# Optimization experiments

Measured on AMD Instinct MI355X. Metric: run time of the kernel, lower is better.

The kernel has to match this reference:

```python
import jax, jax.numpy as jnp
import numpy as np
from jax import lax

DN = ('NCHW', 'OIHW', 'NCHW')

def conv2d(x, w, b):
    y = lax.conv_general_dilated(x, w, (1, 1), 'SAME', dimension_numbers=DN)
    return y + b[None, :, None, None]


def setup_inputs() -> dict:
    key = jax.random.key(0)
    ks = jax.random.split(key, 12)
    B, H, W = 16, 256, 256
    def wt(k, shape):
        return jax.random.normal(k, shape, jnp.float32) * 0.05
    return {
        'x': jax.random.normal(ks[0], (B, 1, H, W), jnp.float32),
        'g': jax.random.normal(ks[1], (B, 1, H, W), jnp.float32),
        # conv1 branch (x): 1->64 relu 64->1
        'w1a': wt(ks[2], (64, 1, 3, 3)), 'b1a': jnp.zeros((64,), jnp.float32),
        'w1b': wt(ks[3], (1, 64, 3, 3)), 'b1b': jnp.zeros((1,), jnp.float32),
        # conv2 branch (g): 1->64 relu 64->1
        'w2a': wt(ks[4], (64, 1, 3, 3)), 'b2a': jnp.zeros((64,), jnp.float32),
        'w2b': wt(ks[5], (1, 64, 3, 3)), 'b2b': jnp.zeros((1,), jnp.float32),
        # dynamic filter head: 2->64 relu 64->64 relu 64->81, softmax over taps
        'wfa': wt(ks[6], (64, 2, 3, 3)), 'bfa': jnp.zeros((64,), jnp.float32),
        'wfb': wt(ks[7], (64, 64, 3, 3)), 'bfb': jnp.zeros((64,), jnp.float32),
        'wfc': wt(ks[8], (81, 64, 3, 3)), 'bfc': jnp.zeros((81,), jnp.float32),
    }


def reference(x, g, w1a, b1a, w1b, b1b, w2a, b2a, w2b, b2b,
              wfa, bfa, wfb, bfb, wfc, bfc):
    # feature branches -> 1 channel each
    x_ = conv2d(jax.nn.relu(conv2d(x, w1a, b1a)), w1b, b1b)   # [B,1,H,W]
    g_ = conv2d(jax.nn.relu(conv2d(g, w2a, b2a)), w2b, b2b)   # [B,1,H,W]
    feat = jnp.concatenate([x_, g_], axis=1)                   # [B,2,H,W]
    # per-pixel 9x9 dynamic filter (81 taps), softmax-normalized
    h = jax.nn.relu(conv2d(feat, wfa, bfa))
    h = jax.nn.relu(conv2d(h, wfb, bfb))
    filt = jax.nn.softmax(conv2d(h, wfc, bfc), axis=1)         # [B,81,H,W]
    # unfold: 9x9 neighborhoods with zero pad 4, row-major tap order
    # matches torch unfold(2,9,1).unfold(3,9,1).permute(0,1,4,5,2,3)
    patches = lax.conv_general_dilated_patches(
        x, (9, 9), (1, 1), padding=((4, 4), (4, 4)),
        dimension_numbers=DN)                                  # [B,81,H,W]
    out = jnp.sum(patches * filt, axis=1, keepdims=True)       # [B,1,H,W]
    return out
```

## Files before the change

kernel.cpp:

```cpp
#include <hip/hip_runtime.h>

#define NB 16
#define HH 256
#define WW 256
#define NPIX (HH*WW)
#define LOG2E 1.44269504088896f

typedef _Float16 f16;
typedef _Float16 f16x8 __attribute__((ext_vector_type(8)));
typedef float f32x4 __attribute__((ext_vector_type(4)));

__device__ __forceinline__ int swzoff(int p, int c) {
    return p * 64 + ((((c >> 3) ^ (p & 7)) << 3) | (c & 7));
}

__global__ __launch_bounds__(256) void prepack_kernel(
    const float* __restrict__ w1a, const float* __restrict__ w2a,
    const float* __restrict__ w1b, const float* __restrict__ w2b,
    const float* __restrict__ wfa, const float* __restrict__ wfb,
    const float* __restrict__ wfc,
    f16* __restrict__ pA1, f16* __restrict__ pA2, f16* __restrict__ pWa,
    f16* __restrict__ pBs1, f16* __restrict__ pBs2,
    f16* __restrict__ pWbF, f16* __restrict__ pWcF)
{
    int i = blockIdx.x * 256 + threadIdx.x;
    if (i < 2048) {
        int c = i >> 5, k = i & 31;
        pA1[i] = (f16)(k < 9 ? w1a[c * 9 + k] : 0.f);
        pA2[i] = (f16)(k < 9 ? w2a[c * 9 + k] : 0.f);
        pWa[i] = (f16)(k < 18 ? wfa[c * 18 + k] : 0.f);
    }
    if (i < 1024) {
        int r = i >> 6, cin = i & 63;
        pBs1[i] = (f16)(r < 9 ? w1b[cin * 9 + r] : 0.f);
        pBs2[i] = (f16)(r < 9 ? w2b[cin * 9 + r] : 0.f);
    }
    if (i < 36864) {
        int kk = i / 2048, r = i & 2047;
        int mt = r >> 9, e = r & 511;
        int l = e >> 3, j = e & 7;
        int cout = mt * 16 + (l & 15);
        int k = kk * 32 + ((l >> 4) << 3) + j;
        int tap = k >> 6, cin = k & 63;
        pWbF[i] = (f16)wfb[(cout * 64 + cin) * 9 + tap];
    }
    if (i < 55296) {
        int kk = i / 3072, r = i % 3072;
        int mt = r >> 9, e = r & 511;
        int l = e >> 3, j = e & 7;
        int cout = mt * 16 + (l & 15);
        int k = kk * 32 + ((l >> 4) << 3) + j;
        int tap = k >> 6, cin = k & 63;
        pWcF[i] = (f16)(cout < 81 ? wfc[(cout * 64 + cin) * 9 + tap] * LOG2E : 0.f);
    }
}

__global__ __launch_bounds__(256, 3) void k1_branch(
    const float* __restrict__ x, const float* __restrict__ g,
    const float* __restrict__ b1a, const float* __restrict__ b2a,
    const float* __restrict__ b1b, const float* __restrict__ b2b,
    const f16* __restrict__ pA1, const f16* __restrict__ pA2,
    const f16* __restrict__ pBs1, const f16* __restrict__ pBs2,
    float* __restrict__ feat)
{
    __shared__ f16 xt[400];
    __shared__ f16 hid[20736];
    __shared__ f16 part[9 * 328];
    __shared__ float bA[64];

    const int tid = threadIdx.x;
    const int wid = tid >> 6, lane = tid & 63;
    const int gq = lane >> 4, cl = lane & 15;
    const int x0 = blockIdx.x * 16, y0 = blockIdx.y * 16;
    const int b = blockIdx.z >> 1, br = blockIdx.z & 1;

    const float* in = (br ? g : x) + (size_t)b * NPIX;
    const f16* pA = br ? pA2 : pA1;
    const f16* pBs = br ? pBs2 : pBs1;
    const float bscal = (br ? b2b : b1b)[0];

    for (int t = tid; t < 400; t += 256) {
        int r = t / 20, c = t % 20;
        int gy = y0 - 2 + r, gx = x0 - 2 + c;
        xt[t] = (f16)(((unsigned)gy < (unsigned)HH && (unsigned)gx < (unsigned)WW)
                          ? in[gy * WW + gx] : 0.f);
    }
    if (tid < 64) bA[tid] = (br ? b2a : b1a)[tid];

    int koff[8];
    #pragma unroll
    for (int j = 0; j < 8; j++) {
        int k = gq * 8 + j;
        int kc = k < 9 ? k : 0;
        koff[j] = (kc / 3) * 20 + (kc % 3);
    }

    f16x8 afA[4];
    #pragma unroll
    for (int mt = 0; mt < 4; mt++)
        afA[mt] = *(const f16x8*)&pA[(mt * 16 + cl) * 32 + gq * 8];
    f16x8 afS0 = *(const f16x8*)&pBs[cl * 64 + gq * 8];
    f16x8 afS1 = *(const f16x8*)&pBs[cl * 64 + 32 + gq * 8];
    __syncthreads();

    #pragma unroll
    for (int it = 0; it < 6; it++) {
        int nt = wid + it * 4;
        if (nt < 21) {
            int p = nt * 16 + cl;
            int pc = p > 323 ? 323 : p;
            int py = pc / 18, px = pc - 18 * py;
            int base = py * 20 + px;
            f16x8 bf;
            #pragma unroll
            for (int j = 0; j < 8; j++) bf[j] = xt[base + koff[j]];
            int gy = y0 - 1 + py, gx = x0 - 1 + px;
            bool ok = (p < 324) &&
                      ((unsigned)gy < (unsigned)HH && (unsigned)gx < (unsigned)WW);
            #pragma unroll
            for (int mt = 0; mt < 4; mt++) {
                f32x4 z = {0.f, 0.f, 0.f, 0.f};
                f32x4 acc = __builtin_amdgcn_mfma_f32_16x16x32_f16(afA[mt], bf, z, 0, 0, 0);
                if (p < 324) {
                    int c0 = mt * 16 + gq * 4;
                    union { f16 h[4]; uint2 u2; } pk;
                    #pragma unroll
                    for (int r = 0; r < 4; r++)
                        pk.h[r] = (f16)(ok ? fmaxf(acc[r] + bA[c0 + r], 0.f) : 0.f);
                    *(uint2*)&hid[swzoff(p, c0)] = pk.u2;
                }
            }
        }
    }
    __syncthreads();

    #pragma unroll
    for (int it = 0; it < 6; it++) {
        int nt = wid + it * 4;
        if (nt < 21) {
            int p = nt * 16 + cl;
            int pc = p > 323 ? 323 : p;
            f16x8 bf0 = *(const f16x8*)&hid[swzoff(pc, gq * 8)];
            f16x8 bf1 = *(const f16x8*)&hid[swzoff(pc, 32 + gq * 8)];
            f32x4 z = {0.f, 0.f, 0.f, 0.f};
            f32x4 d = __builtin_amdgcn_mfma_f32_16x16x32_f16(afS0, bf0, z, 0, 0, 0);
            d = __builtin_amdgcn_mfma_f32_16x16x32_f16(afS1, bf1, d, 0, 0, 0);
            #pragma unroll
            for (int r = 0; r < 4; r++) {
                int tap = gq * 4 + r;
                if (tap < 9 && p < 324)
                    part[tap * 328 + p] = (f16)d[r];
            }
        }
    }
    __syncthreads();

    {
        int ty = tid >> 4, tx = tid & 15;
        float s = bscal;
        #pragma unroll
        for (int u = 0; u < 3; u++)
            #pragma unroll
            for (int v = 0; v < 3; v++)
                s += (float)part[(u * 3 + v) * 328 + (ty + u) * 18 + tx + v];
        feat[((size_t)(b * 2 + br)) * NPIX + (y0 + ty) * WW + x0 + tx] = s;
    }
}

__global__ __launch_bounds__(256, 3) void k2_wfab(
    const float* __restrict__ feat, const f16* __restrict__ pWa,
    const f16* __restrict__ pWbF, const float* __restrict__ bfa,
    const float* __restrict__ bfb, f16* __restrict__ h2g, int b0)
{
    __shared__ f16 ftt[800];
    __shared__ f16 hid[20736];
    __shared__ float bA[64];
    __shared__ float bB[64];

    const int tid = threadIdx.x;
    const int wid = tid >> 6, lane = tid & 63;
    const int gq = lane >> 4, cl = lane & 15;
    const int x0 = blockIdx.x * 16, y0 = blockIdx.y * 16;
    const int ci = blockIdx.z, b = b0 + ci;

    for (int t = tid; t < 800; t += 256) {
        int cin = t / 400, p = t - 400 * cin;
        int r = p / 20, c = p - 20 * r;
        int gy = y0 - 2 + r, gx = x0 - 2 + c;
        ftt[t] = (f16)(((unsigned)gy < (unsigned)HH && (unsigned)gx < (unsigned)WW)
                           ? feat[((size_t)(b * 2 + cin)) * NPIX + gy * WW + gx] : 0.f);
    }
    if (tid < 64) { bA[tid] = bfa[tid]; bB[tid] = bfb[tid]; }

    int koff[8];
    #pragma unroll
    for (int j = 0; j < 8; j++) {
        int k = gq * 8 + j;
        int kc = k < 18 ? k : 0;
        int cin = kc >= 9 ? 1 : 0;
        int tap = kc - 9 * cin;
        koff[j] = cin * 400 + (tap / 3) * 20 + (tap % 3);
    }

    f16x8 afW[4];
    #pragma unroll
    for (int mt = 0; mt < 4; mt++)
        afW[mt] = *(const f16x8*)&pWa[(mt * 16 + cl) * 32 + gq * 8];
    __syncthreads();

    #pragma unroll
    for (int it = 0; it < 6; it++) {
        int nt = wid + it * 4;
        if (nt < 21) {
            int p = nt * 16 + cl;
            int pc = p > 323 ? 323 : p;
            int py = pc / 18, px = pc - 18 * py;
            int base = py * 20 + px;
            f16x8 bf;
            #pragma unroll
            for (int j = 0; j < 8; j++) bf[j] = ftt[base + koff[j]];
            int gy = y0 - 1 + py, gx = x0 - 1 + px;
            bool ok = (p < 324) &&
                      ((unsigned)gy < (unsigned)HH && (unsigned)gx < (unsigned)WW);
            #pragma unroll
            for (int mt = 0; mt < 4; mt++) {
                f32x4 z = {0.f, 0.f, 0.f, 0.f};
                f32x4 acc = __builtin_amdgcn_mfma_f32_16x16x32_f16(afW[mt], bf, z, 0, 0, 0);
                if (p < 324) {
                    int c0 = mt * 16 + gq * 4;
                    union { f16 h[4]; uint2 u2; } pk;
                    #pragma unroll
                    for (int r = 0; r < 4; r++)
                        pk.h[r] = (f16)(ok ? fmaxf(acc[r] + bA[c0 + r], 0.f) : 0.f);
                    *(uint2*)&hid[swzoff(p, c0)] = pk.u2;
                }
            }
        }
    }
    __syncthreads();

    f32x4 acc[4][4];
    #pragma unroll
    for (int i = 0; i < 4; i++)
        #pragma unroll
        for (int mt = 0; mt < 4; mt++) acc[i][mt] = (f32x4){0.f, 0.f, 0.f, 0.f};

    int pre_i[4];
    #pragma unroll
    for (int i = 0; i < 4; i++) pre_i[i] = (wid * 4 + i) * 18 + cl;
    const int A0 = gq * 8;
    const int A1 = 32 + gq * 8;

    const f16* wfp = pWbF + (size_t)lane * 8;
    f16x8 afA[4], afB[4];
    #pragma unroll
    for (int mt = 0; mt < 4; mt++)
        afA[mt] = *(const f16x8*)&wfp[mt * 512];

    #pragma unroll 1
    for (int kt = 0; kt < 9; kt++) {
        int u = kt / 3, duv = u * 18 + (kt - 3 * u);
        #pragma unroll
        for (int mt = 0; mt < 4; mt++)
            afB[mt] = *(const f16x8*)&wfp[((2 * kt + 1) * 4 + mt) * 512];
        #pragma unroll
        for (int i = 0; i < 4; i++) {
            int p = pre_i[i] + duv;
            f16x8 bf = *(const f16x8*)&hid[(p << 6) + (A0 ^ ((p & 7) << 3))];
            __builtin_amdgcn_s_setprio(1);
            #pragma unroll
            for (int mt = 0; mt < 4; mt++)
                acc[i][mt] = __builtin_amdgcn_mfma_f32_16x16x32_f16(afA[mt], bf, acc[i][mt], 0, 0, 0);
            __builtin_amdgcn_s_setprio(0);
        }
        if (kt < 8) {
            #pragma unroll
            for (int mt = 0; mt < 4; mt++)
                afA[mt] = *(const f16x8*)&wfp[((2 * kt + 2) * 4 + mt) * 512];
        }
        #pragma unroll
        for (int i = 0; i < 4; i++) {
            int p = pre_i[i] + duv;
            f16x8 bf = *(const f16x8*)&hid[(p << 6) + (A1 ^ ((p & 7) << 3))];
            __builtin_amdgcn_s_setprio(1);
            #pragma unroll
            for (int mt = 0; mt < 4; mt++)
                acc[i][mt] = __builtin_amdgcn_mfma_f32_16x16x32_f16(afB[mt], bf, acc[i][mt], 0, 0, 0);
            __builtin_amdgcn_s_setprio(0);
        }
    }
    #pragma unroll
    for (int i = 0; i < 4; i++) {
        int nt = wid * 4 + i;
        size_t pb = ((size_t)ci * NPIX + (size_t)((y0 + nt) * WW + x0 + cl)) * 64;
        #pragma unroll
        for (int mt = 0; mt < 4; mt++) {
            int c0 = mt * 16 + gq * 4;
            union { f16 h[4]; uint2 u2; } pk;
            #pragma unroll
            for (int r = 0; r < 4; r++)
                pk.h[r] = (f16)fmaxf(acc[i][mt][r] + bB[c0 + r], 0.f);
            *(uint2*)&h2g[pb + c0] = pk.u2;
        }
    }
}

__global__ __launch_bounds__(256, 3) void k3_wfc_apply(
    const f16* __restrict__ h2g, const f16* __restrict__ pWcF,
    const float* __restrict__ bfc, const float* __restrict__ x,
    float* __restrict__ out, int b0)
{
    __shared__ f16 h2t[20736];
    __shared__ float xt24[576];
    __shared__ float bC[96];

    const int tid = threadIdx.x;
    const int wid = tid >> 6, lane = tid & 63;
    const int gq = lane >> 4, cl = lane & 15;
    const int x0 = blockIdx.x * 16, y0 = blockIdx.y * 16;
    const int ci = blockIdx.z, b = b0 + ci;

    for (int t = tid; t < 2592; t += 256) {
        int p = t >> 3, grp = t & 7;
        int py = p / 18, px = p - 18 * py;
        int gy = y0 - 1 + py, gx = x0 - 1 + px;
        f16x8 v = {};
        if ((unsigned)gy < (unsigned)HH && (unsigned)gx < (unsigned)WW)
            v = *(const f16x8*)&h2g[((size_t)ci * NPIX + (size_t)(gy * WW + gx)) * 64 + grp * 8];
        *(f16x8*)&h2t[swzoff(p, grp * 8)] = v;
    }
    const float* xb = x + (size_t)b * NPIX;
    for (int t = tid; t < 576; t += 256) {
        int r = t / 24, c = t - 24 * r;
        int gy = y0 - 4 + r, gx = x0 - 4 + c;
        xt24[t] = ((unsigned)gy < (unsigned)HH && (unsigned)gx < (unsigned)WW)
                      ? xb[gy * WW + gx] : 0.f;
    }
    if (tid < 96) bC[tid] = tid < 81 ? bfc[tid] * LOG2E : -1e30f;
    __syncthreads();

    f32x4 acc[4][6];
    #pragma unroll
    for (int i = 0; i < 4; i++)
        #pragma unroll
        for (int mt = 0; mt < 6; mt++) acc[i][mt] = (f32x4){0.f, 0.f, 0.f, 0.f};

    int pre_i[4];
    #pragma unroll
    for (int i = 0; i < 4; i++) pre_i[i] = (wid * 4 + i) * 18 + cl;
    const int A0 = gq * 8;
    const int A1 = 32 + gq * 8;

    const f16* wfp = pWcF + (size_t)lane * 8;
    f16x8 afA[6], afB[6];
    #pragma unroll
    for (int mt = 0; mt < 6; mt++)
        afA[mt] = *(const f16x8*)&wfp[mt * 512];

    #pragma unroll 1
    for (int kt = 0; kt < 9; kt++) {
        int u = kt / 3, duv = u * 18 + (kt - 3 * u);
        #pragma unroll
        for (int mt = 0; mt < 6; mt++)
            afB[mt] = *(const f16x8*)&wfp[((2 * kt + 1) * 6 + mt) * 512];
        #pragma unroll
        for (int i = 0; i < 4; i++) {
            int p = pre_i[i] + duv;
            f16x8 bf = *(const f16x8*)&h2t[(p << 6) + (A0 ^ ((p & 7) << 3))];
            __builtin_amdgcn_s_setprio(1);
            #pragma unroll
            for (int mt = 0; mt < 6; mt++)
                acc[i][mt] = __builtin_amdgcn_mfma_f32_16x16x32_f16(afA[mt], bf, acc[i][mt], 0, 0, 0);
            __builtin_amdgcn_s_setprio(0);
        }
        if (kt < 8) {
            #pragma unroll
            for (int mt = 0; mt < 6; mt++)
                afA[mt] = *(const f16x8*)&wfp[((2 * kt + 2) * 6 + mt) * 512];
        }
        #pragma unroll
        for (int i = 0; i < 4; i++) {
            int p = pre_i[i] + duv;
            f16x8 bf = *(const f16x8*)&h2t[(p << 6) + (A1 ^ ((p & 7) << 3))];
            __builtin_amdgcn_s_setprio(1);
            #pragma unroll
            for (int mt = 0; mt < 6; mt++)
                acc[i][mt] = __builtin_amdgcn_mfma_f32_16x16x32_f16(afB[mt], bf, acc[i][mt], 0, 0, 0);
            __builtin_amdgcn_s_setprio(0);
        }
    }

    int xoff[6][4];
    #pragma unroll
    for (int mt = 0; mt < 6; mt++)
        #pragma unroll
        for (int r = 0; r < 4; r++) {
            int c = mt * 16 + gq * 4 + r;
            xoff[mt][r] = (c / 9) * 24 + (c % 9);
        }

    #pragma unroll
    for (int i = 0; i < 4; i++) {
        int nt = wid * 4 + i;
        int xbase = nt * 24 + cl;
        float val[6][4];
        float m = -1e30f;
        #pragma unroll
        for (int mt = 0; mt < 6; mt++)
            #pragma unroll
            for (int r = 0; r < 4; r++) {
                int c = mt * 16 + gq * 4 + r;
                float vv = acc[i][mt][r] + bC[c];
                val[mt][r] = vv;
                m = fmaxf(m, vv);
            }
        m = fmaxf(m, __shfl_xor(m, 16));
        m = fmaxf(m, __shfl_xor(m, 32));
        float s = 0.f, o = 0.f;
        #pragma unroll
        for (int mt = 0; mt < 6; mt++)
            #pragma unroll
            for (int r = 0; r < 4; r++) {
                float e = __builtin_amdgcn_exp2f(val[mt][r] - m);
                s += e;
                o += e * xt24[xbase + xoff[mt][r]];
            }
        s += __shfl_xor(s, 16); s += __shfl_xor(s, 32);
        o += __shfl_xor(o, 16); o += __shfl_xor(o, 32);
        if (gq == 0)
            out[(size_t)b * NPIX + (y0 + nt) * WW + x0 + cl] = o / s;
    }
}

extern "C" void kernel_launch(void* const* d_in, const int* in_sizes, int n_in,
                              void* d_out, int out_size, void* d_ws, size_t ws_size,
                              hipStream_t stream)
{
    const float* x   = (const float*)d_in[0];
    const float* g   = (const float*)d_in[1];
    const float* w1a = (const float*)d_in[2];  const float* b1a = (const float*)d_in[3];
    const float* w1b = (const float*)d_in[4];  const float* b1b = (const float*)d_in[5];
    const float* w2a = (const float*)d_in[6];  const float* b2a = (const float*)d_in[7];
    const float* w2b = (const float*)d_in[8];  const float* b2b = (const float*)d_in[9];
    const float* wfa = (const float*)d_in[10]; const float* bfa = (const float*)d_in[11];
    const float* wfb = (const float*)d_in[12]; const float* bfb = (const float*)d_in[13];
    const float* wfc = (const float*)d_in[14]; const float* bfc = (const float*)d_in[15];
    float* out = (float*)d_out;

    float* feat = (float*)d_ws;
    size_t featB = 2097152ull * 4;
    size_t pkB = 100352ull * 2;
    int nbc = 16;
    while (nbc > 1 && featB + (size_t)nbc * NPIX * 64 * 2 + pkB > ws_size) nbc >>= 1;

    f16* h2g = (f16*)((char*)d_ws + featB);
    f16* pk  = h2g + (size_t)nbc * NPIX * 64;
    f16* pA1  = pk;
    f16* pA2  = pA1 + 2048;
    f16* pWa  = pA2 + 2048;
    f16* pBs1 = pWa + 2048;
    f16* pBs2 = pBs1 + 1024;
    f16* pWbF = pBs2 + 1024;
    f16* pWcF = pWbF + 36864;

    prepack_kernel<<<dim3(216), 256, 0, stream>>>(
        w1a, w2a, w1b, w2b, wfa, wfb, wfc, pA1, pA2, pWa, pBs1, pBs2, pWbF, pWcF);

    k1_branch<<<dim3(16, 16, 32), 256, 0, stream>>>(
        x, g, b1a, b2a, b1b, b2b, pA1, pA2, pBs1, pBs2, feat);

    for (int b0 = 0; b0 < NB; b0 += nbc) {
        int cn = (NB - b0) < nbc ? (NB - b0) : nbc;
        k2_wfab<<<dim3(16, 16, cn), 256, 0, stream>>>(
            feat, pWa, pWbF, bfa, bfb, h2g, b0);
        k3_wfc_apply<<<dim3(16, 16, cn), 256, 0, stream>>>(
            h2g, pWcF, bfc, x, out, b0);
    }
}
```

Measured before the change: 326.3 us.

## Fuse wfb and wfc conv stages into one head kernel with halo recompute

Merges the wfa/wfb kernel and the wfc+softmax+apply kernel into one 512-thread kernel. The 64-channel second hidden layer stays in shared memory instead of going through a large global fp16 buffer. Each tile now recomputes the first hidden layer over a 20x20 halo, in three row strips, and the second layer over an 18x18 halo. The aim is to remove the global write and read of h2 and one kernel launch. The cost is redundant halo compute, more barriers, idle waves in some phases and higher shared-memory use per block.

New measurement: 466.0 us. +42.8%, slower.

```diff
diff --git a/kernel.cpp b/kernel.cpp
--- a/kernel.cpp
+++ b/kernel.cpp
@@ -167,30 +167,44 @@
     }
 }
 
-__global__ __launch_bounds__(256, 3) void k2_wfab(
+__global__ __launch_bounds__(512, 4) void k23_head(
     const float* __restrict__ feat, const f16* __restrict__ pWa,
-    const f16* __restrict__ pWbF, const float* __restrict__ bfa,
-    const float* __restrict__ bfb, f16* __restrict__ h2g, int b0)
+    const f16* __restrict__ pWbF, const f16* __restrict__ pWcF,
+    const float* __restrict__ bfa, const float* __restrict__ bfb,
+    const float* __restrict__ bfc, const float* __restrict__ x,
+    float* __restrict__ out)
 {
-    __shared__ f16 ftt[800];
-    __shared__ f16 hid[20736];
+    __shared__ f16 ftt[968];
+    __shared__ f16 h1S[180 * 64];
+    __shared__ f16 h2t[324 * 64];
+    __shared__ float xt24[576];
     __shared__ float bA[64];
     __shared__ float bB[64];
+    __shared__ float bC[96];
 
     const int tid = threadIdx.x;
     const int wid = tid >> 6, lane = tid & 63;
     const int gq = lane >> 4, cl = lane & 15;
     const int x0 = blockIdx.x * 16, y0 = blockIdx.y * 16;
-    const int ci = blockIdx.z, b = b0 + ci;
-
-    for (int t = tid; t < 800; t += 256) {
-        int cin = t / 400, p = t - 400 * cin;
-        int r = p / 20, c = p - 20 * r;
-        int gy = y0 - 2 + r, gx = x0 - 2 + c;
+    const int b = blockIdx.z;
+
+    for (int t = tid; t < 968; t += 512) {
+        int cin = t / 484, p = t - 484 * cin;
+        int r = p / 22, c = p - 22 * r;
+        int gy = y0 - 3 + r, gx = x0 - 3 + c;
         ftt[t] = (f16)(((unsigned)gy < (unsigned)HH && (unsigned)gx < (unsigned)WW)
                            ? feat[((size_t)(b * 2 + cin)) * NPIX + gy * WW + gx] : 0.f);
     }
+    const float* xb = x + (size_t)b * NPIX;
+    for (int t = tid; t < 576; t += 512) {
+        int r = t / 24, c = t - 24 * r;
+        int gy = y0 - 4 + r, gx = x0 - 4 + c;
+        xt24[t] = ((unsigned)gy < (unsigned)HH && (unsigned)gx < (unsigned)WW)
+                      ? xb[gy * WW + gx] : 0.f;
+    }
     if (tid < 64) { bA[tid] = bfa[tid]; bB[tid] = bfb[tid]; }
+    if (tid >= 64 && tid < 160)
+        bC[tid - 64] = (tid - 64) < 81 ? bfc[tid - 64] * LOG2E : -1e30f;
 
     int koff[8];
     #pragma unroll
@@ -199,193 +213,157 @@
         int kc = k < 18 ? k : 0;
         int cin = kc >= 9 ? 1 : 0;
         int tap = kc - 9 * cin;
-        koff[j] = cin * 400 + (tap / 3) * 20 + (tap % 3);
-    }
-
+        koff[j] = cin * 484 + (tap / 3) * 22 + (tap % 3);
+    }
     f16x8 afW[4];
     #pragma unroll
     for (int mt = 0; mt < 4; mt++)
         afW[mt] = *(const f16x8*)&pWa[(mt * 16 + cl) * 32 + gq * 8];
     __syncthreads();
 
-    #pragma unroll
-    for (int it = 0; it < 6; it++) {
-        int nt = wid + it * 4;
-        if (nt < 21) {
-            int p = nt * 16 + cl;
-            int pc = p > 323 ? 323 : p;
-            int py = pc / 18, px = pc - 18 * py;
-            int base = py * 20 + px;
+    const int A0 = gq * 8;
+    const int A1 = 32 + gq * 8;
+    const f16* wfpB = pWbF + (size_t)lane * 8;
+
+    #pragma unroll 1
+    for (int s = 0; s < 3; s++) {
+        const int base1 = s * 6;
+        const int cnt = (s == 2) ? 160 : 180;
+        const int nit = (s == 2) ? 10 : 12;
+
+        #pragma unroll 1
+        for (int it = wid; it < nit; it += 8) {
+            int idx = it * 16 + cl;
+            int ic = idx >= cnt ? cnt - 1 : idx;
+            int lr = ic / 20, c1 = ic - 20 * lr;
+            int r1 = base1 + lr;
+            int bse = r1 * 22 + c1;
             f16x8 bf;
             #pragma unroll
-            for (int j = 0; j < 8; j++) bf[j] = ftt[base + koff[j]];
-            int gy = y0 - 1 + py, gx = x0 - 1 + px;
-            bool ok = (p < 324) &&
+            for (int j = 0; j < 8; j++) bf[j] = ftt[bse + koff[j]];
+            int gy = y0 + r1 - 2, gx = x0 + c1 - 2;
+            bool ok = (idx < cnt) &&
                       ((unsigned)gy < (unsigned)HH && (unsigned)gx < (unsigned)WW);
             #pragma unroll
             for (int mt = 0; mt < 4; mt++) {
                 f32x4 z = {0.f, 0.f, 0.f, 0.f};
-                f32x4 acc = __builtin_amdgcn_mfma_f32_16x16x32_f16(afW[mt], bf, z, 0, 0, 0);
-                if (p < 324) {
+                f32x4 a = __builtin_amdgcn_mfma_f32_16x16x32_f16(afW[mt], bf, z, 0, 0, 0);
+                if (idx < cnt) {
                     int c0 = mt * 16 + gq * 4;
                     union { f16 h[4]; uint2 u2; } pk;
                     #pragma unroll
                     for (int r = 0; r < 4; r++)
-                        pk.h[r] = (f16)(ok ? fmaxf(acc[r] + bA[c0 + r], 0.f) : 0.f);
-                    *(uint2*)&hid[swzoff(p, c0)] = pk.u2;
-                }
-            }
-        }
-    }
-    __syncthreads();
-
-    f32x4 acc[4][4];
-    #pragma unroll
-    for (int i = 0; i < 4; i++)
-        #pragma unroll
-        for (int mt = 0; mt < 4; mt++) acc[i][mt] = (f32x4){0.f, 0.f, 0.f, 0.f};
-
-    int pre_i[4];
-    #pragma unroll
-    for (int i = 0; i < 4; i++) pre_i[i] = (wid * 4 + i) * 18 + cl;
-    const int A0 = gq * 8;
-    const int A1 = 32 + gq * 8;
-
-    const f16* wfp = pWbF + (size_t)lane * 8;
-    f16x8 afA[4], afB[4];
-    #pragma unroll
-    for (int mt = 0; mt < 4; mt++)
-        afA[mt] = *(const f16x8*)&wfp[mt * 512];
+                        pk.h[r] = (f16)(ok ? fmaxf(a[r] + bA[c0 + r], 0.f) : 0.f);
+                    *(uint2*)&h1S[swzoff(idx, c0)] = pk.u2;
+                }
+            }
+        }
+        __syncthreads();
+
+        {
+            int qm = 7 * s + (wid < 7 ? wid : 6);
+            int q = qm * 16 + cl;
+            int pc = q > 323 ? 323 : q;
+            int fr = pc / 18, fc = pc - 18 * fr;
+            int lbase = (fr - base1) * 20 + fc;
+            f32x4 acc[4];
+            #pragma unroll
+            for (int mt = 0; mt < 4; mt++) acc[mt] = (f32x4){0.f, 0.f, 0.f, 0.f};
+            f16x8 afA[4], afB[4];
+            #pragma unroll
+            for (int mt = 0; mt < 4; mt++)
+                afA[mt] = *(const f16x8*)&wfpB[mt * 512];
+            #pragma unroll 1
+            for (int kt = 0; kt < 9; kt++) {
+                int u = kt / 3, duv = u * 20 + (kt - 3 * u);
+                #pragma unroll
+                for (int mt = 0; mt < 4; mt++)
+                    afB[mt] = *(const f16x8*)&wfpB[((2 * kt + 1) * 4 + mt) * 512];
+                int lp = lbase + duv;
+                {
+                    f16x8 bf = *(const f16x8*)&h1S[(lp << 6) + (A0 ^ ((lp & 7) << 3))];
+                    __builtin_amdgcn_s_setprio(1);
+                    #pragma unroll
+                    for (int mt = 0; mt < 4; mt++)
+                        acc[mt] = __builtin_amdgcn_mfma_f32_16x16x32_f16(afA[mt], bf, acc[mt], 0, 0, 0);
+                    __builtin_amdgcn_s_setprio(0);
+                }
+                if (kt < 8) {
+                    #pragma unroll
+                    for (int mt = 0; mt < 4; mt++)
+                        afA[mt] = *(const f16x8*)&wfpB[((2 * kt + 2) * 4 + mt) * 512];
+                }
+                {
+                    f16x8 bf = *(const f16x8*)&h1S[(lp << 6) + (A1 ^ ((lp & 7) << 3))];
+                    __builtin_amdgcn_s_setprio(1);
+                    #pragma unroll
+                    for (int mt = 0; mt < 4; mt++)
+                        acc[mt] = __builtin_amdgcn_mfma_f32_16x16x32_f16(afB[mt], bf, acc[mt], 0, 0, 0);
+                    __builtin_amdgcn_s_setprio(0);
+                }
+            }
+            int gy = y0 + fr - 1, gx = x0 + fc - 1;
+            bool inimg = ((unsigned)gy < (unsigned)HH && (unsigned)gx < (unsigned)WW);
+            if (wid < 7 && q <= 323) {
+                #pragma unroll
+                for (int mt = 0; mt < 4; mt++) {
+                    int c0 = mt * 16 + gq * 4;
+                    union { f16 h[4]; uint2 u2; } pk;
+                    #pragma unroll
+                    for (int r = 0; r < 4; r++)
+                        pk.h[r] = (f16)(inimg ? fmaxf(acc[mt][r] + bB[c0 + r], 0.f) : 0.f);
+                    *(uint2*)&h2t[swzoff(pc, c0)] = pk.u2;
+                }
+            }
+        }
+        __syncthreads();
+    }
+
+    f32x4 acc[2][6];
+    #pragma unroll
+    for (int i = 0; i < 2; i++)
+        #pragma unroll
+        for (int mt = 0; mt < 6; mt++) acc[i][mt] = (f32x4){0.f, 0.f, 0.f, 0.f};
+
+    int pre_i[2];
+    #pragma unroll
+    for (int i = 0; i < 2; i++) pre_i[i] = (wid * 2 + i) * 18 + cl;
+
+    const f16* wfpC = pWcF + (size_t)lane * 8;
+    f16x8 cfA[6], cfB[6];
+    #pragma unroll
+    for (int mt = 0; mt < 6; mt++)
+        cfA[mt] = *(const f16x8*)&wfpC[mt * 512];
 
     #pragma unroll 1
     for (int kt = 0; kt < 9; kt++) {
         int u = kt / 3, duv = u * 18 + (kt - 3 * u);
         #pragma unroll
-        for (int mt = 0; mt < 4; mt++)
-            afB[mt] = *(const f16x8*)&wfp[((2 * kt + 1) * 4 + mt) * 512];
-        #pragma unroll
-        for (int i = 0; i < 4; i++) {
-            int p = pre_i[i] + duv;
-            f16x8 bf = *(const f16x8*)&hid[(p << 6) + (A0 ^ ((p & 7) << 3))];
-            __builtin_amdgcn_s_setprio(1);
-            #pragma unroll
-            for (int mt = 0; mt < 4; mt++)
-                acc[i][mt] = __builtin_amdgcn_mfma_f32_16x16x32_f16(afA[mt], bf, acc[i][mt], 0, 0, 0);
-            __builtin_amdgcn_s_setprio(0);
-        }
-        if (kt < 8) {
-            #pragma unroll
-            for (int mt = 0; mt < 4; mt++)
-                afA[mt] = *(const f16x8*)&wfp[((2 * kt + 2) * 4 + mt) * 512];
-        }
-        #pragma unroll
-        for (int i = 0; i < 4; i++) {
-            int p = pre_i[i] + duv;
-            f16x8 bf = *(const f16x8*)&hid[(p << 6) + (A1 ^ ((p & 7) << 3))];
-            __builtin_amdgcn_s_setprio(1);
-            #pragma unroll
-            for (int mt = 0; mt < 4; mt++)
-                acc[i][mt] = __builtin_amdgcn_mfma_f32_16x16x32_f16(afB[mt], bf, acc[i][mt], 0, 0, 0);
-            __builtin_amdgcn_s_setprio(0);
-        }
-    }
-    #pragma unroll
-    for (int i = 0; i < 4; i++) {
-        int nt = wid * 4 + i;
-        size_t pb = ((size_t)ci * NPIX + (size_t)((y0 + nt) * WW + x0 + cl)) * 64;
-        #pragma unroll
-        for (int mt = 0; mt < 4; mt++) {
-            int c0 = mt * 16 + gq * 4;
-            union { f16 h[4]; uint2 u2; } pk;
-            #pragma unroll
-            for (int r = 0; r < 4; r++)
-                pk.h[r] = (f16)fmaxf(acc[i][mt][r] + bB[c0 + r], 0.f);
-            *(uint2*)&h2g[pb + c0] = pk.u2;
-        }
-    }
-}
-
-__global__ __launch_bounds__(256, 3) void k3_wfc_apply(
-    const f16* __restrict__ h2g, const f16* __restrict__ pWcF,
-    const float* __restrict__ bfc, const float* __restrict__ x,
-    float* __restrict__ out, int b0)
-{
-    __shared__ f16 h2t[20736];
-    __shared__ float xt24[576];
-    __shared__ float bC[96];
-
-    const int tid = threadIdx.x;
-    const int wid = tid >> 6, lane = tid & 63;
-    const int gq = lane >> 4, cl = lane & 15;
-    const int x0 = blockIdx.x * 16, y0 = blockIdx.y * 16;
-    const int ci = blockIdx.z, b = b0 + ci;
-
-    for (int t = tid; t < 2592; t += 256) {
-        int p = t >> 3, grp = t & 7;
-        int py = p / 18, px = p - 18 * py;
-        int gy = y0 - 1 + py, gx = x0 - 1 + px;
-        f16x8 v = {};
-        if ((unsigned)gy < (unsigned)HH && (unsigned)gx < (unsigned)WW)
-            v = *(const f16x8*)&h2g[((size_t)ci * NPIX + (size_t)(gy * WW + gx)) * 64 + grp * 8];
-        *(f16x8*)&h2t[swzoff(p, grp * 8)] = v;
-    }
-    const float* xb = x + (size_t)b * NPIX;
-    for (int t = tid; t < 576; t += 256) {
-        int r = t / 24, c = t - 24 * r;
-        int gy = y0 - 4 + r, gx = x0 - 4 + c;
-        xt24[t] = ((unsigned)gy < (unsigned)HH && (unsigned)gx < (unsigned)WW)
-                      ? xb[gy * WW + gx] : 0.f;
-    }
-    if (tid < 96) bC[tid] = tid < 81 ? bfc[tid] * LOG2E : -1e30f;
-    __syncthreads();
-
-    f32x4 acc[4][6];
-    #pragma unroll
-    for (int i = 0; i < 4; i++)
-        #pragma unroll
-        for (int mt = 0; mt < 6; mt++) acc[i][mt] = (f32x4){0.f, 0.f, 0.f, 0.f};
-
-    int pre_i[4];
-    #pragma unroll
-    for (int i = 0; i < 4; i++) pre_i[i] = (wid * 4 + i) * 18 + cl;
-    const int A0 = gq * 8;
-    const int A1 = 32 + gq * 8;
-
-    const f16* wfp = pWcF + (size_t)lane * 8;
-    f16x8 afA[6], afB[6];
-    #pragma unroll
-    for (int mt = 0; mt < 6; mt++)
-        afA[mt] = *(const f16x8*)&wfp[mt * 512];
-
-    #pragma unroll 1
-    for (int kt = 0; kt < 9; kt++) {
-        int u = kt / 3, duv = u * 18 + (kt - 3 * u);
-        #pragma unroll
         for (int mt = 0; mt < 6; mt++)
-            afB[mt] = *(const f16x8*)&wfp[((2 * kt + 1) * 6 + mt) * 512];
-        #pragma unroll
-        for (int i = 0; i < 4; i++) {
+            cfB[mt] = *(const f16x8*)&wfpC[((2 * kt + 1) * 6 + mt) * 512];
+        #pragma unroll
+        for (int i = 0; i < 2; i++) {
             int p = pre_i[i] + duv;
             f16x8 bf = *(const f16x8*)&h2t[(p << 6) + (A0 ^ ((p & 7) << 3))];
             __builtin_amdgcn_s_setprio(1);
             #pragma unroll
             for (int mt = 0; mt < 6; mt++)
-                acc[i][mt] = __builtin_amdgcn_mfma_f32_16x16x32_f16(afA[mt], bf, acc[i][mt], 0, 0, 0);
+                acc[i][mt] = __builtin_amdgcn_mfma_f32_16x16x32_f16(cfA[mt], bf, acc[i][mt], 0, 0, 0);
             __builtin_amdgcn_s_setprio(0);
         }
         if (kt < 8) {
             #pragma unroll
             for (int mt = 0; mt < 6; mt++)
-                afA[mt] = *(const f16x8*)&wfp[((2 * kt + 2) * 6 + mt) * 512];
-        }
-        #pragma unroll
-        for (int i = 0; i < 4; i++) {
+                cfA[mt] = *(const f16x8*)&wfpC[((2 * kt + 2) * 6 + mt) * 512];
+        }
+        #pragma unroll
+        for (int i = 0; i < 2; i++) {
             int p = pre_i[i] + duv;
             f16x8 bf = *(const f16x8*)&h2t[(p << 6) + (A1 ^ ((p & 7) << 3))];
             __builtin_amdgcn_s_setprio(1);
             #pragma unroll
             for (int mt = 0; mt < 6; mt++)
-                acc[i][mt] = __builtin_amdgcn_mfma_f32_16x16x32_f16(afB[mt], bf, acc[i][mt], 0, 0, 0);
+                acc[i][mt] = __builtin_amdgcn_mfma_f32_16x16x32_f16(cfB[mt], bf, acc[i][mt], 0, 0, 0);
             __builtin_amdgcn_s_setprio(0);
         }
     }
@@ -400,8 +378,8 @@
         }
 
     #pragma unroll
-    for (int i = 0; i < 4; i++) {
-        int nt = wid * 4 + i;
+    for (int i = 0; i < 2; i++) {
+        int nt = wid * 2 + i;
         int xbase = nt * 24 + cl;
         float val[6][4];
         float m = -1e30f;
@@ -448,14 +426,7 @@
     float* out = (float*)d_out;
 
     float* feat = (float*)d_ws;
-    size_t featB = 2097152ull * 4;
-    size_t pkB = 100352ull * 2;
-    int nbc = 16;
-    while (nbc > 1 && featB + (size_t)nbc * NPIX * 64 * 2 + pkB > ws_size) nbc >>= 1;
-
-    f16* h2g = (f16*)((char*)d_ws + featB);
-    f16* pk  = h2g + (size_t)nbc * NPIX * 64;
-    f16* pA1  = pk;
+    f16* pA1  = (f16*)(feat + 2097152);
     f16* pA2  = pA1 + 2048;
     f16* pWa  = pA2 + 2048;
     f16* pBs1 = pWa + 2048;
@@ -469,11 +440,6 @@
     k1_branch<<<dim3(16, 16, 32), 256, 0, stream>>>(
         x, g, b1a, b2a, b1b, b2b, pA1, pA2, pBs1, pBs2, feat);
 
-    for (int b0 = 0; b0 < NB; b0 += nbc) {
-        int cn = (NB - b0) < nbc ? (NB - b0) : nbc;
-        k2_wfab<<<dim3(16, 16, cn), 256, 0, stream>>>(
-            feat, pWa, pWbF, bfa, bfb, h2g, b0);
-        k3_wfc_apply<<<dim3(16, 16, cn), 256, 0, stream>>>(
-            h2g, pWcF, bfc, x, out, b0);
-    }
+    k23_head<<<dim3(16, 16, NB), 512, 0, stream>>>(
+        feat, pWa, pWbF, pWcF, bfa, bfb, bfc, x, out);
 }
```
